# Performance work log

Measured on AMD Instinct MI355X. Metric: run time of the kernel, lower is better.

The kernel has to match this reference:

```python
import jax, jax.numpy as jnp
import numpy as np


def setup_inputs() -> dict:
    key = jax.random.key(0)
    k0, k1, k2, k3 = jax.random.split(key, 4)
    B, T, K = 1024, 1024, 32
    inputs = jax.random.normal(k0, (B, T, K), dtype=jnp.float32)
    mask = jnp.ones((B, T), dtype=bool)  # mask[:, 0] must be all True for CRF
    # torchcrf initializes all transition params uniform in [-0.1, 0.1]
    start_transitions = jax.random.uniform(k1, (K,), minval=-0.1, maxval=0.1, dtype=jnp.float32)
    end_transitions = jax.random.uniform(k2, (K,), minval=-0.1, maxval=0.1, dtype=jnp.float32)
    transitions = jax.random.uniform(k3, (K, K), minval=-0.1, maxval=0.1, dtype=jnp.float32)
    return {
        "inputs": inputs,
        "mask": mask,
        "start_transitions": start_transitions,
        "end_transitions": end_transitions,
        "transitions": transitions,
    }


def reference(inputs, mask, start_transitions, end_transitions, transitions):
    """CRF Viterbi decode (torchcrf.CRF.decode), vectorized over batch.

    inputs: [B, T, K] emissions; mask: [B, T] bool. Returns best tag path [B, T] int32.
    """
    em = jnp.swapaxes(inputs, 0, 1)  # [T, B, K] (time-major, as torchcrf internally)
    mk = jnp.swapaxes(mask, 0, 1)    # [T, B]

    score0 = start_transitions[None, :] + em[0]  # [B, K]

    def fwd_step(score, xs):
        em_t, m_t = xs
        # cand[b, i, j] = score[b, i] + transitions[i, j] + em_t[b, j]
        cand = score[:, :, None] + transitions[None, :, :] + em_t[:, None, :]  # [B, K, K]
        bp = jnp.argmax(cand, axis=1).astype(jnp.int32)  # [B, K] backpointers
        new_score = jnp.max(cand, axis=1)                # [B, K]
        score = jnp.where(m_t[:, None], new_score, score)
        return score, bp

    score, hist = jax.lax.scan(fwd_step, score0, (em[1:], mk[1:]))  # hist: [T-1, B, K]
    score = score + end_transitions[None, :]
    last_tag = jnp.argmax(score, axis=1).astype(jnp.int32)  # [B]

    def back_step(tag, xs):
        bp, m_t = xs  # bp: [B, K], m_t: [B]
        prev = jnp.take_along_axis(bp, tag[:, None], axis=1)[:, 0]
        prev = jnp.where(m_t, prev, tag)  # masked step: position did not advance
        return prev, tag

    first_tag, rest = jax.lax.scan(back_step, last_tag, (hist[::-1], mk[1:][::-1]))
    tags = jnp.concatenate([first_tag[None, :], rest[::-1]], axis=0)  # [T, B]
    return jnp.swapaxes(tags, 0, 1)  # [B, T]
```

## Files before the change

### kernel.cpp

```cpp
#include <hip/hip_runtime.h>
#include <stdint.h>

#define BB 1024
#define TT 1024
#define KK 32

typedef unsigned u32x2 __attribute__((ext_vector_type(2)));

#define ADDDPP(d, s, t, RR)                                                     \
    asm("v_add_f32_dpp %0, %1, %2 row_ror:" #RR " row_mask:0xf bank_mask:0xf"   \
        : "=v"(d) : "v"(s), "v"(t))

__device__ __forceinline__ float fm3(float a, float b, float c) { return fmaxf(fmaxf(a, b), c); }
__device__ __forceinline__ unsigned um3(unsigned a, unsigned b, unsigned c) {
    unsigned m = a < b ? a : b; return m < c ? m : c;
}
__device__ __forceinline__ unsigned umin2(unsigned a, unsigned b) { return a < b ? a : b; }

template <int X>
__device__ __forceinline__ void bfly(float& val, int& idx) {
    float sv = __int_as_float(__builtin_amdgcn_ds_swizzle(__float_as_int(val), (X << 10) | 0x1F));
    int si = __builtin_amdgcn_ds_swizzle(idx, (X << 10) | 0x1F);
    bool better = (sv > val) || ((sv == val) && (si < idx));
    val = better ? sv : val;
    idx = better ? si : idx;
}

#define VSTEP(K_, PF_)                                                          \
    {                                                                           \
        float emv = e[K_];                                                      \
        float x[16];                                                            \
        x[0] = score + trA[0];                                                  \
        ADDDPP(x[1], score, trA[1], 1);                                         \
        ADDDPP(x[2], score, trA[2], 2);                                         \
        ADDDPP(x[3], score, trA[3], 3);                                         \
        ADDDPP(x[4], score, trA[4], 4);                                         \
        ADDDPP(x[5], score, trA[5], 5);                                         \
        ADDDPP(x[6], score, trA[6], 6);                                         \
        ADDDPP(x[7], score, trA[7], 7);                                         \
        ADDDPP(x[8], score, trA[8], 8);                                         \
        ADDDPP(x[9], score, trA[9], 9);                                         \
        ADDDPP(x[10], score, trA[10], 10);                                      \
        ADDDPP(x[11], score, trA[11], 11);                                      \
        ADDDPP(x[12], score, trA[12], 12);                                      \
        ADDDPP(x[13], score, trA[13], 13);                                      \
        ADDDPP(x[14], score, trA[14], 14);                                      \
        ADDDPP(x[15], score, trA[15], 15);                                      \
        float m0 = fm3(x[0], x[1], x[2]);                                       \
        float m1 = fm3(x[3], x[4], x[5]);                                       \
        float m2 = fm3(x[6], x[7], x[8]);                                       \
        float m3 = fm3(x[9], x[10], x[11]);                                     \
        float m4 = fm3(x[12], x[13], x[14]);                                    \
        float best = fmaxf(fm3(m0, m1, m2), fm3(m3, m4, x[15]));                \
        u32x2 bb = __builtin_amdgcn_permlane32_swap(                            \
            (unsigned)__float_as_int(best), (unsigned)__float_as_int(best),     \
            false, false);                                                      \
        float nv = fmaxf(__int_as_float((int)bb[0]), __int_as_float((int)bb[1])); \
        float sc = nv + emv;                                                    \
        if (P == ((1 + K_) & 1)) {                                              \
            unsigned tq[16];                                                    \
            _Pragma("unroll")                                                   \
            for (int r = 0; r < 16; ++r) {                                      \
                float cr = x[r] + emv;                                          \
                tq[r] = (cr == sc) ? i16[r] : 63u;                              \
            }                                                                   \
            unsigned n0 = um3(tq[0], tq[1], tq[2]);                             \
            unsigned n1 = um3(tq[3], tq[4], tq[5]);                             \
            unsigned n2 = um3(tq[6], tq[7], tq[8]);                             \
            unsigned n3 = um3(tq[9], tq[10], tq[11]);                           \
            unsigned n4 = um3(tq[12], tq[13], tq[14]);                          \
            unsigned lr = umin2(um3(n0, n1, n2), um3(n3, n4, tq[15]));          \
            unsigned gidx = lr + (unsigned)sbase;                               \
            u32x2 gg = __builtin_amdgcn_permlane32_swap(gidx, gidx, false, false); \
            unsigned ni = umin2(gg[0], gg[1]);                                  \
            bpb[bpo + K_ * 32] = (uint8_t)ni;                                   \
        }                                                                       \
        u32x2 ssw = __builtin_amdgcn_permlane16_swap(                           \
            (unsigned)__float_as_int(sc), (unsigned)__float_as_int(sc),         \
            false, false);                                                      \
        float partner = __int_as_float((int)(ssw[0] ^ ssw[1] ^ (unsigned)__float_as_int(sc))); \
        score = pb ? partner : sc;                                              \
        if (PF_) e[K_] = emB[eo + K_ * 32];                                     \
    }

__global__ void __launch_bounds__(64) crf_forward(
    const float* __restrict__ em,
    const float* __restrict__ start_t,
    const float* __restrict__ end_t,
    const float* __restrict__ trans,
    uint8_t* __restrict__ bp,
    int* __restrict__ last_tag,
    int* __restrict__ out)
{
    const int P = (int)(blockIdx.x & 1);
    const int b = (int)(blockIdx.x >> 1);
    const int lane = threadIdx.x;
    const int col = lane & 15;
    const int row = lane >> 4;
    const int S = row >> 1;
    const int sbase = S << 4;
    const int pb = (row == 1 || row == 2) ? 1 : 0;
    const int joff = col + ((row & 1) << 4);
    const int hidx = col + sbase;

    unsigned i16[16];
#pragma unroll
    for (int r = 0; r < 16; ++r) i16[r] = (unsigned)((col - r) & 15);

    float trA[16];
#pragma unroll
    for (int r = 0; r < 16; ++r) trA[r] = trans[(sbase + (int)i16[r]) * KK + joff];

    const float* emB = em + (size_t)b * TT * KK;
    uint8_t* bpb = bp + (size_t)b * TT * KK;

    float score = start_t[hidx] + emB[hidx];
    if (P == 0) bpb[joff] = (uint8_t)joff;

    float e[6];
#pragma unroll
    for (int k = 0; k < 6; ++k) e[k] = emB[(1 + k) * KK + joff];

    unsigned bpo = KK + joff;
    unsigned eo = 7 * KK + joff;

    for (int it = 0; it < 169; ++it) {
        VSTEP(0, 1) VSTEP(1, 1) VSTEP(2, 1) VSTEP(3, 1) VSTEP(4, 1) VSTEP(5, 1)
        bpo += 192; eo += 192;
    }
    VSTEP(0, 1) VSTEP(1, 1) VSTEP(2, 1) VSTEP(3, 0) VSTEP(4, 0) VSTEP(5, 0)
    bpo += 192;
    VSTEP(0, 0) VSTEP(1, 0) VSTEP(2, 0)

    if (P == 0) {
        float val = score + end_t[hidx];
        int idx = hidx;
        bfly<1>(val, idx); bfly<2>(val, idx); bfly<4>(val, idx); bfly<8>(val, idx);
        {
            u32x2 pv2 = __builtin_amdgcn_permlane32_swap(
                (unsigned)__float_as_int(val), (unsigned)__float_as_int(val), false, false);
            int pix2 = (int)(pv2[0] ^ pv2[1] ^ (unsigned)__float_as_int(val));
            float pv = __int_as_float(pix2);
            u32x2 pi2 = __builtin_amdgcn_permlane32_swap((unsigned)idx, (unsigned)idx, false, false);
            int pix = (int)(pi2[0] ^ pi2[1] ^ (unsigned)idx);
            bool bt = (pv > val) || ((pv == val) && (pix < idx));
            val = bt ? pv : val;
            idx = bt ? pix : idx;
        }
        if (lane == 0) {
            last_tag[b] = idx;
            out[b * TT + (TT - 1)] = idx;
        }
    }
}

__global__ void __launch_bounds__(256) crf_chunkmap(const uint8_t* __restrict__ bp,
                                                    uint8_t* __restrict__ map) {
    int tid = threadIdx.x;
    int w = blockIdx.x * 8 + (tid >> 5);
    int b = w >> 4, c = w & 15, e = tid & 31;
    const uint8_t* bpb = bp + (size_t)b * TT * KK;
    int cur = e;
    int lo = c * 64;
#pragma unroll 4
    for (int t = lo + 63; t >= lo; --t) cur = bpb[t * KK + cur];
    map[(w << 5) + e] = (uint8_t)cur;
}

__global__ void __launch_bounds__(256) crf_stitch(const uint8_t* __restrict__ map,
                                                  const int* __restrict__ last_tag,
                                                  uint8_t* __restrict__ chosen) {
    int b = blockIdx.x * 256 + threadIdx.x;
    int e = last_tag[b];
    chosen[b * 16 + 15] = (uint8_t)e;
    for (int c = 15; c >= 1; --c) {
        e = map[(b * 16 + c) * 32 + e];
        chosen[b * 16 + c - 1] = (uint8_t)e;
    }
}

__global__ void __launch_bounds__(256) crf_emit(const uint8_t* __restrict__ bp,
                                                const uint8_t* __restrict__ chosen,
                                                int* __restrict__ out) {
    int w = blockIdx.x * 256 + threadIdx.x;
    int b = w >> 4, c = w & 15;
    const uint8_t* bpb = bp + (size_t)b * TT * KK;
    int cur = chosen[w];
    int* ob = out + b * TT;
    int lo = c * 64;
    for (int t = lo + 63; t >= lo; --t) {
        cur = bpb[t * KK + cur];
        if (t >= 1) ob[t - 1] = cur;
    }
}

extern "C" void kernel_launch(void* const* d_in, const int* in_sizes, int n_in,
                              void* d_out, int out_size, void* d_ws, size_t ws_size,
                              hipStream_t stream) {
    (void)in_sizes; (void)n_in; (void)out_size;
    const float* em      = (const float*)d_in[0];
    const float* start_t = (const float*)d_in[2];
    const float* end_t   = (const float*)d_in[3];
    const float* trans   = (const float*)d_in[4];
    int* out = (int*)d_out;

    char* ws = (char*)d_ws;
    (void)ws_size;
    int* last_tag   = (int*)ws;
    uint8_t* bp     = (uint8_t*)(ws + 4096);
    uint8_t* map    = bp + (size_t)BB * TT * KK;
    uint8_t* chosen = map + (size_t)BB * 16 * 32;

    crf_forward<<<BB * 2, 64, 0, stream>>>(em, start_t, end_t, trans, bp, last_tag, out);
    crf_chunkmap<<<2048, 256, 0, stream>>>(bp, map);
    crf_stitch<<<4, 256, 0, stream>>>(map, last_tag, chosen);
    crf_emit<<<64, 256, 0, stream>>>(bp, chosen, out);
}
```

Baseline: 306.7 us.

## Use one block per batch row and stage backpointers in LDS for 16-byte stores

Measured after the change: 325.2 us. +6.1%, slower.

```diff
diff --git a/kernel.cpp b/kernel.cpp
--- a/kernel.cpp
+++ b/kernel.cpp
@@ -26,9 +26,9 @@
     idx = better ? si : idx;
 }
 
-#define VSTEP(K_, PF_)                                                          \
+#define VSTEP(S_, PF_)                                                          \
     {                                                                           \
-        float emv = e[K_];                                                      \
+        float emv = e[S_];                                                      \
         float x[16];                                                            \
         x[0] = score + trA[0];                                                  \
         ADDDPP(x[1], score, trA[1], 1);                                         \
@@ -57,31 +57,40 @@
             false, false);                                                      \
         float nv = fmaxf(__int_as_float((int)bb[0]), __int_as_float((int)bb[1])); \
         float sc = nv + emv;                                                    \
-        if (P == ((1 + K_) & 1)) {                                              \
-            unsigned tq[16];                                                    \
-            _Pragma("unroll")                                                   \
-            for (int r = 0; r < 16; ++r) {                                      \
-                float cr = x[r] + emv;                                          \
-                tq[r] = (cr == sc) ? i16[r] : 63u;                              \
-            }                                                                   \
-            unsigned n0 = um3(tq[0], tq[1], tq[2]);                             \
-            unsigned n1 = um3(tq[3], tq[4], tq[5]);                             \
-            unsigned n2 = um3(tq[6], tq[7], tq[8]);                             \
-            unsigned n3 = um3(tq[9], tq[10], tq[11]);                           \
-            unsigned n4 = um3(tq[12], tq[13], tq[14]);                          \
-            unsigned lr = umin2(um3(n0, n1, n2), um3(n3, n4, tq[15]));          \
-            unsigned gidx = lr + (unsigned)sbase;                               \
-            u32x2 gg = __builtin_amdgcn_permlane32_swap(gidx, gidx, false, false); \
-            unsigned ni = umin2(gg[0], gg[1]);                                  \
-            bpb[bpo + K_ * 32] = (uint8_t)ni;                                   \
+        unsigned tq[16];                                                        \
+        _Pragma("unroll")                                                       \
+        for (int r = 0; r < 16; ++r) {                                          \
+            float cr = x[r] + emv;                                              \
+            tq[r] = (cr == sc) ? i16[r] : 63u;                                  \
         }                                                                       \
+        unsigned n0 = um3(tq[0], tq[1], tq[2]);                                 \
+        unsigned n1 = um3(tq[3], tq[4], tq[5]);                                 \
+        unsigned n2 = um3(tq[6], tq[7], tq[8]);                                 \
+        unsigned n3 = um3(tq[9], tq[10], tq[11]);                               \
+        unsigned n4 = um3(tq[12], tq[13], tq[14]);                              \
+        unsigned lr = umin2(um3(n0, n1, n2), um3(n3, n4, tq[15]));              \
+        unsigned gidx = lr + (unsigned)sbase;                                   \
+        u32x2 gg = __builtin_amdgcn_permlane32_swap(gidx, gidx, false, false);  \
+        unsigned ni = umin2(gg[0], gg[1]);                                      \
+        if (row2) bpbuf[((S_) << 5) + joff] = (uint8_t)ni;                      \
         u32x2 ssw = __builtin_amdgcn_permlane16_swap(                           \
             (unsigned)__float_as_int(sc), (unsigned)__float_as_int(sc),         \
             false, false);                                                      \
-        float partner = __int_as_float((int)(ssw[0] ^ ssw[1] ^ (unsigned)__float_as_int(sc))); \
-        score = pb ? partner : sc;                                              \
-        if (PF_) e[K_] = emB[eo + K_ * 32];                                     \
-    }
+        score = pb ? __int_as_float((int)(ssw[0] ^ ssw[1] ^ (unsigned)__float_as_int(sc))) : sc; \
+        if (PF_) e[S_] = emB[eo + (S_) * 32];                                   \
+    }
+
+#define FLUSH(G_)                                                               \
+    if (row2) {                                                                 \
+        uint4 fv = *(const uint4*)&bpbuf[((lane >> 1) << 5) + ((lane & 1) << 4)]; \
+        *(uint4*)(bpb + ((unsigned)(G_) << 9) + (lane << 4)) = fv;              \
+    }
+
+#define STEP16(PF_)                                                             \
+    VSTEP(0, PF_) VSTEP(1, PF_) VSTEP(2, PF_) VSTEP(3, PF_)                     \
+    VSTEP(4, PF_) VSTEP(5, PF_) VSTEP(6, PF_) VSTEP(7, PF_)                     \
+    VSTEP(8, PF_) VSTEP(9, PF_) VSTEP(10, PF_) VSTEP(11, PF_)                   \
+    VSTEP(12, PF_) VSTEP(13, PF_) VSTEP(14, PF_) VSTEP(15, PF_)
 
 __global__ void __launch_bounds__(64) crf_forward(
     const float* __restrict__ em,
@@ -92,16 +101,18 @@
     int* __restrict__ last_tag,
     int* __restrict__ out)
 {
-    const int P = (int)(blockIdx.x & 1);
-    const int b = (int)(blockIdx.x >> 1);
+    const int b = blockIdx.x;
     const int lane = threadIdx.x;
     const int col = lane & 15;
     const int row = lane >> 4;
     const int S = row >> 1;
     const int sbase = S << 4;
     const int pb = (row == 1 || row == 2) ? 1 : 0;
+    const bool row2 = (row < 2);
     const int joff = col + ((row & 1) << 4);
     const int hidx = col + sbase;
+
+    __shared__ __align__(16) uint8_t bpbuf[512];
 
     unsigned i16[16];
 #pragma unroll
@@ -115,42 +126,47 @@
     uint8_t* bpb = bp + (size_t)b * TT * KK;
 
     float score = start_t[hidx] + emB[hidx];
-    if (P == 0) bpb[joff] = (uint8_t)joff;
-
-    float e[6];
+    if (row2) bpbuf[joff] = (uint8_t)joff;
+
+    float e[16];
 #pragma unroll
-    for (int k = 0; k < 6; ++k) e[k] = emB[(1 + k) * KK + joff];
-
-    unsigned bpo = KK + joff;
-    unsigned eo = 7 * KK + joff;
-
-    for (int it = 0; it < 169; ++it) {
-        VSTEP(0, 1) VSTEP(1, 1) VSTEP(2, 1) VSTEP(3, 1) VSTEP(4, 1) VSTEP(5, 1)
-        bpo += 192; eo += 192;
-    }
-    VSTEP(0, 1) VSTEP(1, 1) VSTEP(2, 1) VSTEP(3, 0) VSTEP(4, 0) VSTEP(5, 0)
-    bpo += 192;
-    VSTEP(0, 0) VSTEP(1, 0) VSTEP(2, 0)
-
-    if (P == 0) {
-        float val = score + end_t[hidx];
-        int idx = hidx;
-        bfly<1>(val, idx); bfly<2>(val, idx); bfly<4>(val, idx); bfly<8>(val, idx);
-        {
-            u32x2 pv2 = __builtin_amdgcn_permlane32_swap(
-                (unsigned)__float_as_int(val), (unsigned)__float_as_int(val), false, false);
-            int pix2 = (int)(pv2[0] ^ pv2[1] ^ (unsigned)__float_as_int(val));
-            float pv = __int_as_float(pix2);
-            u32x2 pi2 = __builtin_amdgcn_permlane32_swap((unsigned)idx, (unsigned)idx, false, false);
-            int pix = (int)(pi2[0] ^ pi2[1] ^ (unsigned)idx);
-            bool bt = (pv > val) || ((pv == val) && (pix < idx));
-            val = bt ? pv : val;
-            idx = bt ? pix : idx;
-        }
-        if (lane == 0) {
-            last_tag[b] = idx;
-            out[b * TT + (TT - 1)] = idx;
-        }
+    for (int k = 0; k < 16; ++k) e[k] = emB[k * KK + joff];
+
+    unsigned eo = 16 * KK + joff;
+
+    VSTEP(1, 1) VSTEP(2, 1) VSTEP(3, 1) VSTEP(4, 1) VSTEP(5, 1) VSTEP(6, 1)
+    VSTEP(7, 1) VSTEP(8, 1) VSTEP(9, 1) VSTEP(10, 1) VSTEP(11, 1) VSTEP(12, 1)
+    VSTEP(13, 1) VSTEP(14, 1) VSTEP(15, 1)
+    e[0] = emB[eo];
+    FLUSH(0)
+    eo += 512;
+
+    for (int g = 1; g < 63; ++g) {
+        STEP16(1)
+        FLUSH(g)
+        eo += 512;
+    }
+
+    STEP16(0)
+    FLUSH(63)
+
+    float val = score + end_t[hidx];
+    int idx = hidx;
+    bfly<1>(val, idx); bfly<2>(val, idx); bfly<4>(val, idx); bfly<8>(val, idx);
+    {
+        u32x2 pv2 = __builtin_amdgcn_permlane32_swap(
+            (unsigned)__float_as_int(val), (unsigned)__float_as_int(val), false, false);
+        int pix2 = (int)(pv2[0] ^ pv2[1] ^ (unsigned)__float_as_int(val));
+        float pv = __int_as_float(pix2);
+        u32x2 pi2 = __builtin_amdgcn_permlane32_swap((unsigned)idx, (unsigned)idx, false, false);
+        int pix = (int)(pi2[0] ^ pi2[1] ^ (unsigned)idx);
+        bool bt = (pv > val) || ((pv == val) && (pix < idx));
+        val = bt ? pv : val;
+        idx = bt ? pix : idx;
+    }
+    if (lane == 0) {
+        last_tag[b] = idx;
+        out[b * TT + (TT - 1)] = idx;
     }
 }
 
@@ -211,7 +227,7 @@
     uint8_t* map    = bp + (size_t)BB * TT * KK;
     uint8_t* chosen = map + (size_t)BB * 16 * 32;
 
-    crf_forward<<<BB * 2, 64, 0, stream>>>(em, start_t, end_t, trans, bp, last_tag, out);
+    crf_forward<<<BB, 64, 0, stream>>>(em, start_t, end_t, trans, bp, last_tag, out);
     crf_chunkmap<<<2048, 256, 0, stream>>>(bp, map);
     crf_stitch<<<4, 256, 0, stream>>>(map, last_tag, chosen);
     crf_emit<<<64, 256, 0, stream>>>(bp, chosen, out);
```
